# Performance work log

Measured on AMD Instinct MI355X. Metric: run time of the kernel, lower is better.

Reference implementation:

```python
import jax, jax.numpy as jnp
import numpy as np

B, N, E = 4, 8192, 1024
H, G = 16, 64            # num_heads, num_groups
D = E // H               # head_dim = 64
GS = N // G              # group (block) size = 128


def setup_inputs() -> dict:
    key = jax.random.key(0)
    ks = jax.random.split(key, 11)
    std = 0.02
    mk = lambda k, shape: (jax.random.normal(k, shape, dtype=jnp.float32) * std)
    return {
        "q": jax.random.normal(ks[0], (B, N, E), dtype=jnp.float32),
        "k": jax.random.normal(ks[1], (B, N, E), dtype=jnp.float32),
        "v": jax.random.normal(ks[2], (B, N, E), dtype=jnp.float32),
        "Wq": mk(ks[3], (E, E)), "bq": jnp.zeros((E,), jnp.float32),
        "Wk": mk(ks[4], (E, E)), "bk": jnp.zeros((E,), jnp.float32),
        "Wv": mk(ks[5], (E, E)), "bv": jnp.zeros((E,), jnp.float32),
        "Wo": mk(ks[6], (E, E)), "bo": jnp.zeros((E,), jnp.float32),
    }


def reference(q, k, v, Wq, bq, Wk, bk, Wv, bv, Wo, bo):
    b, n, e = q.shape
    scale = 1.0 / (D ** 0.5)

    def proj(x, W, bias):
        # [b,n,e] -> [b,H,G,GS,D]  (split heads, then split seq into groups)
        y = x @ W + bias
        return y.reshape(b, n, H, D).transpose(0, 2, 1, 3).reshape(b, H, G, GS, D)

    qh = proj(q, Wq, bq)
    kh = proj(k, Wk, bk)
    vh = proj(v, Wv, bv)

    # block-diagonal attention: each seq group attends only within itself
    scores = jnp.einsum('bhgqd,bhgkd->bhgqk', qh, kh) * scale  # [b,H,G,GS,GS]
    w = jax.nn.softmax(scores, axis=-1)
    og = jnp.einsum('bhgqk,bhgkd->bhgqd', w, vh)               # [b,H,G,GS,D]

    out = og.reshape(b, H, n, D).transpose(0, 2, 1, 3).reshape(b, n, e)
    out = out @ Wo + bo
    # torch version returns attn_weights of the last group from the loop
    return out, w[:, :, -1]
```

## Files before the change

### kernel.cpp

```cpp
#include <hip/hip_runtime.h>
#include <stdint.h>

#define DEVI static __device__ __forceinline__

typedef __attribute__((ext_vector_type(8))) __bf16 bf16x8;
typedef __attribute__((ext_vector_type(4))) float f32x4;

#define MFMA16(a, b, c) __builtin_amdgcn_mfma_f32_16x16x32_bf16((a), (b), (c), 0, 0, 0)

DEVI uint16_t f2bf(float f) {
  uint32_t u = __builtin_bit_cast(uint32_t, f);
  u += 0x7fffu + ((u >> 16) & 1u);
  return (uint16_t)(u >> 16);
}

DEVI void gload16(const void* g, void* l) {
  __builtin_amdgcn_global_load_lds((const __attribute__((address_space(1))) void*)g,
                                   (__attribute__((address_space(3))) void*)l, 16, 0, 0);
}

#define BARRIER()                         \
  do {                                    \
    __builtin_amdgcn_sched_barrier(0);    \
    __builtin_amdgcn_s_barrier();         \
    __builtin_amdgcn_sched_barrier(0);    \
  } while (0)

__global__ __launch_bounds__(256) void cvt_bf16(const float* __restrict__ in,
                                                uint16_t* __restrict__ out, long n) {
  long i = ((long)blockIdx.x * 256 + threadIdx.x) * 8;
  if (i >= n) return;
  float4 a = *(const float4*)(in + i);
  float4 b = *(const float4*)(in + i + 4);
  union { uint16_t u[8]; uint4 v; } r;
  r.u[0] = f2bf(a.x); r.u[1] = f2bf(a.y); r.u[2] = f2bf(a.z); r.u[3] = f2bf(a.w);
  r.u[4] = f2bf(b.x); r.u[5] = f2bf(b.y); r.u[6] = f2bf(b.z); r.u[7] = f2bf(b.w);
  *(uint4*)(out + i) = r.v;
}

__global__ __launch_bounds__(256) void wtrans(const float* __restrict__ W,
                                              uint16_t* __restrict__ Wt) {
  __shared__ float t[64][65];
  const int ti = blockIdx.y * 64, tj = blockIdx.x * 64;
  {
    int r = threadIdx.x >> 2, c0 = (threadIdx.x & 3) * 16;
#pragma unroll
    for (int i = 0; i < 16; i += 4) {
      float4 v = *(const float4*)(W + (size_t)(ti + r) * 1024 + tj + c0 + i);
      t[r][c0 + i + 0] = v.x; t[r][c0 + i + 1] = v.y;
      t[r][c0 + i + 2] = v.z; t[r][c0 + i + 3] = v.w;
    }
  }
  __syncthreads();
  {
    int c = threadIdx.x >> 2, r0 = (threadIdx.x & 3) * 16;
    union { uint16_t u[16]; uint4 v[2]; } b;
#pragma unroll
    for (int i = 0; i < 16; ++i) b.u[i] = f2bf(t[r0 + i][c]);
    uint16_t* dst = Wt + (size_t)(tj + c) * 1024 + ti + r0;
    *(uint4*)dst = b.v[0];
    *(uint4*)(dst + 8) = b.v[1];
  }
}

__global__ __launch_bounds__(512, 2) void gemm256(const uint16_t* __restrict__ A,
                                                  const uint16_t* __restrict__ Bt,
                                                  const float* __restrict__ bias,
                                                  void* __restrict__ C, int cf32) {
  __shared__ uint8_t lds[131072];
  const int tid = threadIdx.x;
  const int l = tid & 63, w = tid >> 6;
  const int wr = w >> 2, wc = w & 3;
  const int lc = l & 15, lq = l >> 4;

  const int bid = blockIdx.y * 4 + blockIdx.x;
  const int swz = (bid & 7) * 64 + (bid >> 3);
  const size_t m0 = (size_t)(swz >> 2) * 256;
  const int n0 = (swz & 3) * 256;

  const uint8_t* Ab = (const uint8_t*)A + m0 * 2048;
  const uint8_t* Bb = (const uint8_t*)Bt + (size_t)n0 * 2048;

  const int crow = l >> 2;
  const int csw = 16 * ((l & 3) ^ ((l >> 3) & 3));

  auto stageA = [&](int sb, int kt) {
#pragma unroll
    for (int j = 0; j < 2; ++j) {
      const int c = w * 2 + j;
      gload16(Ab + (size_t)(c * 16 + crow) * 2048 + kt * 64 + csw,
              lds + sb * 16384 + c * 1024);
    }
  };
  auto stageB = [&](int sb, int kt) {
#pragma unroll
    for (int j = 0; j < 2; ++j) {
      const int c = w * 2 + j;
      gload16(Bb + (size_t)(c * 16 + crow) * 2048 + kt * 64 + csw,
              lds + 65536 + sb * 16384 + c * 1024);
    }
  };

  const int sel = ((lc >> 1) & 3) << 4;
  auto ldsA = [&](int bf, int mi) -> bf16x8 {
    const int row = wr * 128 + mi * 16 + lc;
    return *(const bf16x8*)(lds + bf * 16384 + row * 64 + ((lq * 16) ^ sel));
  };
  auto ldsB = [&](int bf, int ni) -> bf16x8 {
    const int row = wc * 64 + ni * 16 + lc;
    return *(const bf16x8*)(lds + 65536 + bf * 16384 + row * 64 + ((lq * 16) ^ sel));
  };

  f32x4 acc[8][4] = {};
  bf16x8 aF[8], bF[4];

  stageA(0, 0); stageB(0, 0);
  stageA(1, 1); stageB(1, 1);
  stageA(2, 2); stageB(2, 2);
  asm volatile("s_waitcnt vmcnt(8)" ::: "memory");
  BARRIER();

  for (int kt = 0; kt < 32; ++kt) {
    const int bf = kt & 3;
    const int sb = (kt + 3) & 3;
    const bool st = (kt + 3) < 32;

    if (st) stageA(sb, kt + 3);
#pragma unroll
    for (int mi = 0; mi < 8; ++mi) aF[mi] = ldsA(bf, mi);
#pragma unroll
    for (int ni = 0; ni < 2; ++ni) bF[ni] = ldsB(bf, ni);
    __builtin_amdgcn_s_setprio(1);
#pragma unroll
    for (int mi = 0; mi < 8; ++mi)
#pragma unroll
      for (int ni = 0; ni < 2; ++ni)
        acc[mi][ni] = MFMA16(aF[mi], bF[ni], acc[mi][ni]);
    __builtin_amdgcn_s_setprio(0);

    if (st) stageB(sb, kt + 3);
#pragma unroll
    for (int ni = 2; ni < 4; ++ni) bF[ni] = ldsB(bf, ni);
    __builtin_amdgcn_s_setprio(1);
#pragma unroll
    for (int mi = 0; mi < 8; ++mi)
#pragma unroll
      for (int ni = 2; ni < 4; ++ni)
        acc[mi][ni] = MFMA16(aF[mi], bF[ni], acc[mi][ni]);
    __builtin_amdgcn_s_setprio(0);

    if (kt < 29)       { asm volatile("s_waitcnt vmcnt(8)" ::: "memory"); }
    else if (kt == 29) { asm volatile("s_waitcnt vmcnt(4)" ::: "memory"); }
    else if (kt == 30) { asm volatile("s_waitcnt vmcnt(0)" ::: "memory"); }
    if (kt < 31) BARRIER();
  }

#pragma unroll
  for (int mi = 0; mi < 8; ++mi) {
#pragma unroll
    for (int ni = 0; ni < 4; ++ni) {
      const int col = n0 + wc * 64 + ni * 16 + lc;
      const float bb = bias[col];
#pragma unroll
      for (int r = 0; r < 4; ++r) {
        const size_t row = m0 + wr * 128 + mi * 16 + lq * 4 + r;
        const float vv = acc[mi][ni][r] + bb;
        if (cf32) ((float*)C)[row * 1024 + col] = vv;
        else      ((uint16_t*)C)[row * 1024 + col] = f2bf(vv);
      }
    }
  }
}

__global__ __launch_bounds__(256) void attn(const uint16_t* __restrict__ Qh,
                                            const uint16_t* __restrict__ Kh,
                                            const uint16_t* __restrict__ Vh,
                                            uint16_t* __restrict__ Oh,
                                            float* __restrict__ Wlast) {
  __shared__ uint16_t Ks[128][72];
  __shared__ uint16_t Vt[64][136];
  __shared__ uint16_t Ps[128][136];

  const int blk = blockIdx.x;
  const int b = blk >> 10;
  const int h = (blk >> 6) & 15;
  const int g = blk & 63;
  const size_t rowbase = (size_t)b * 8192 + (size_t)g * 128;
  const int colbase = h * 64;

  const int tid = threadIdx.x, lane = tid & 63, wv = tid >> 6;
  const int lc = lane & 15, lq = lane >> 4;
  const int m0 = wv * 32;

  {
    const int r = tid >> 1, hf = (tid & 1) * 32;
    const uint16_t* ksrc = Kh + (rowbase + r) * 1024 + colbase + hf;
    const uint16_t* vsrc = Vh + (rowbase + r) * 1024 + colbase + hf;
    union { uint16_t u[32]; uint4 v[4]; } kk, vb;
#pragma unroll
    for (int i = 0; i < 4; ++i) kk.v[i] = *(const uint4*)(ksrc + i * 8);
#pragma unroll
    for (int i = 0; i < 4; ++i) vb.v[i] = *(const uint4*)(vsrc + i * 8);
#pragma unroll
    for (int i = 0; i < 4; ++i) *(uint4*)&Ks[r][hf + i * 8] = kk.v[i];
#pragma unroll
    for (int j = 0; j < 32; ++j) Vt[hf + j][r] = vb.u[j];
  }

  bf16x8 aq[2][2];
#pragma unroll
  for (int mi = 0; mi < 2; ++mi)
#pragma unroll
    for (int ks = 0; ks < 2; ++ks)
      aq[mi][ks] = *(const bf16x8*)(Qh + (rowbase + m0 + mi * 16 + lc) * 1024 +
                                    colbase + ks * 32 + lq * 8);

  __syncthreads();

  f32x4 sacc[2][8] = {};
#pragma unroll
  for (int ks = 0; ks < 2; ++ks) {
#pragma unroll
    for (int ni = 0; ni < 8; ++ni) {
      bf16x8 bk = *(const bf16x8*)&Ks[ni * 16 + lc][ks * 32 + lq * 8];
      sacc[0][ni] = MFMA16(aq[0][ks], bk, sacc[0][ni]);
      sacc[1][ni] = MFMA16(aq[1][ks], bk, sacc[1][ni]);
    }
  }

  const float scale = 0.125f;
  float mx[2][4], sm[2][4];
#pragma unroll
  for (int mi = 0; mi < 2; ++mi)
#pragma unroll
    for (int r = 0; r < 4; ++r) {
      float m = -1e30f;
#pragma unroll
      for (int ni = 0; ni < 8; ++ni) m = fmaxf(m, sacc[mi][ni][r]);
      m = fmaxf(m, __shfl_xor(m, 1));
      m = fmaxf(m, __shfl_xor(m, 2));
      m = fmaxf(m, __shfl_xor(m, 4));
      m = fmaxf(m, __shfl_xor(m, 8));
      mx[mi][r] = m * scale;
    }
#pragma unroll
  for (int mi = 0; mi < 2; ++mi)
#pragma unroll
    for (int ni = 0; ni < 8; ++ni)
#pragma unroll
      for (int r = 0; r < 4; ++r)
        sacc[mi][ni][r] = __expf(sacc[mi][ni][r] * scale - mx[mi][r]);
#pragma unroll
  for (int mi = 0; mi < 2; ++mi)
#pragma unroll
    for (int r = 0; r < 4; ++r) {
      float s = 0.f;
#pragma unroll
      for (int ni = 0; ni < 8; ++ni) s += sacc[mi][ni][r];
      s += __shfl_xor(s, 1); s += __shfl_xor(s, 2);
      s += __shfl_xor(s, 4); s += __shfl_xor(s, 8);
      sm[mi][r] = 1.0f / s;
    }

#pragma unroll
  for (int mi = 0; mi < 2; ++mi)
#pragma unroll
    for (int ni = 0; ni < 8; ++ni)
#pragma unroll
      for (int r = 0; r < 4; ++r) {
        float wgt = sacc[mi][ni][r] * sm[mi][r];
        sacc[mi][ni][r] = wgt;
        Ps[m0 + mi * 16 + lq * 4 + r][ni * 16 + lc] = f2bf(wgt);
      }
  if (g == 63) {
    float* wl = Wlast + (size_t)(b * 16 + h) * 16384;
#pragma unroll
    for (int mi = 0; mi < 2; ++mi)
#pragma unroll
      for (int ni = 0; ni < 8; ++ni)
#pragma unroll
        for (int r = 0; r < 4; ++r)
          wl[(size_t)(m0 + mi * 16 + lq * 4 + r) * 128 + ni * 16 + lc] =
              sacc[mi][ni][r];
  }
  __syncthreads();

  f32x4 oacc[2][4] = {};
#pragma unroll
  for (int ks = 0; ks < 4; ++ks) {
    bf16x8 ap[2], bq[4];
#pragma unroll
    for (int mi = 0; mi < 2; ++mi)
      ap[mi] = *(const bf16x8*)&Ps[m0 + mi * 16 + lc][ks * 32 + lq * 8];
#pragma unroll
    for (int ni = 0; ni < 4; ++ni)
      bq[ni] = *(const bf16x8*)&Vt[ni * 16 + lc][ks * 32 + lq * 8];
#pragma unroll
    for (int mi = 0; mi < 2; ++mi)
#pragma unroll
      for (int ni = 0; ni < 4; ++ni)
        oacc[mi][ni] = MFMA16(ap[mi], bq[ni], oacc[mi][ni]);
  }
#pragma unroll
  for (int mi = 0; mi < 2; ++mi)
#pragma unroll
    for (int ni = 0; ni < 4; ++ni)
#pragma unroll
      for (int r = 0; r < 4; ++r)
        Oh[(rowbase + m0 + mi * 16 + lq * 4 + r) * 1024 + colbase + ni * 16 + lc] =
            f2bf(oacc[mi][ni][r]);
}

extern "C" void kernel_launch(void* const* d_in, const int* in_sizes, int n_in,
                              void* d_out, int out_size, void* d_ws, size_t ws_size,
                              hipStream_t stream) {
  (void)in_sizes; (void)n_in; (void)out_size; (void)ws_size;
  const float* q  = (const float*)d_in[0];
  const float* k  = (const float*)d_in[1];
  const float* v  = (const float*)d_in[2];
  const float* Wq = (const float*)d_in[3];
  const float* bq = (const float*)d_in[4];
  const float* Wk = (const float*)d_in[5];
  const float* bk = (const float*)d_in[6];
  const float* Wv = (const float*)d_in[7];
  const float* bv = (const float*)d_in[8];
  const float* Wo = (const float*)d_in[9];
  const float* bo = (const float*)d_in[10];

  uint8_t* ws = (uint8_t*)d_ws;
  const size_t WSZ = (size_t)1024 * 1024 * 2;
  const size_t TSZ = (size_t)32768 * 1024 * 2;
  uint16_t* Wtq = (uint16_t*)(ws + 0 * WSZ);
  uint16_t* Wtk = (uint16_t*)(ws + 1 * WSZ);
  uint16_t* Wtv = (uint16_t*)(ws + 2 * WSZ);
  uint16_t* Wto = (uint16_t*)(ws + 3 * WSZ);
  uint16_t* Qh  = (uint16_t*)(ws + 4 * WSZ);
  uint16_t* Khp = (uint16_t*)(ws + 4 * WSZ + 1 * TSZ);
  uint16_t* Vhp = (uint16_t*)(ws + 4 * WSZ + 2 * TSZ);
  uint16_t* Xs  = (uint16_t*)(ws + 4 * WSZ + 3 * TSZ);

  dim3 tb(256);
  wtrans<<<dim3(16, 16), tb, 0, stream>>>(Wq, Wtq);
  wtrans<<<dim3(16, 16), tb, 0, stream>>>(Wk, Wtk);
  wtrans<<<dim3(16, 16), tb, 0, stream>>>(Wv, Wtv);
  wtrans<<<dim3(16, 16), tb, 0, stream>>>(Wo, Wto);

  const long NE = (long)32768 * 1024;
  const dim3 gg(4, 128), gb(512);
  cvt_bf16<<<16384, tb, 0, stream>>>(q, Xs, NE);
  gemm256<<<gg, gb, 0, stream>>>(Xs, Wtq, bq, Qh, 0);
  cvt_bf16<<<16384, tb, 0, stream>>>(k, Xs, NE);
  gemm256<<<gg, gb, 0, stream>>>(Xs, Wtk, bk, Khp, 0);
  cvt_bf16<<<16384, tb, 0, stream>>>(v, Xs, NE);
  gemm256<<<gg, gb, 0, stream>>>(Xs, Wtv, bv, Vhp, 0);

  float* outp = (float*)d_out;
  attn<<<4096, tb, 0, stream>>>(Qh, Khp, Vhp, Xs, outp + (size_t)32768 * 1024);
  gemm256<<<gg, gb, 0, stream>>>(Xs, Wto, bo, outp, 1);
}
```

Measured before the change: 499.2 us.

## Fuse fp32-to-bf16 conversion into batched QKV projection GEMM, double-buffer LDS

Drops the separate cvt_bf16 passes: the projection GEMM now reads fp32 activations straight from global memory, converts them to bf16 in registers and writes them into swizzled LDS. The Q, K and V projections run as one launch with a z grid dimension, and the four weight transposes are merged into one launch. The GEMM pipeline shrinks from a 4-stage async LDS ring to a 2-stage double buffer with register-staged A, which halves LDS use but exposes more load latency through full vmcnt(0) waits on every iteration. An unused stub kernel gemm256_3 is also left in the file.

```diff
diff --git a/kernel.cpp b/kernel.cpp
--- a/kernel.cpp
+++ b/kernel.cpp
@@ -26,21 +26,15 @@
     __builtin_amdgcn_sched_barrier(0);    \
   } while (0)
 
-__global__ __launch_bounds__(256) void cvt_bf16(const float* __restrict__ in,
-                                                uint16_t* __restrict__ out, long n) {
-  long i = ((long)blockIdx.x * 256 + threadIdx.x) * 8;
-  if (i >= n) return;
-  float4 a = *(const float4*)(in + i);
-  float4 b = *(const float4*)(in + i + 4);
-  union { uint16_t u[8]; uint4 v; } r;
-  r.u[0] = f2bf(a.x); r.u[1] = f2bf(a.y); r.u[2] = f2bf(a.z); r.u[3] = f2bf(a.w);
-  r.u[4] = f2bf(b.x); r.u[5] = f2bf(b.y); r.u[6] = f2bf(b.z); r.u[7] = f2bf(b.w);
-  *(uint4*)(out + i) = r.v;
-}
-
-__global__ __launch_bounds__(256) void wtrans(const float* __restrict__ W,
-                                              uint16_t* __restrict__ Wt) {
+struct W4 {
+  const float* W[4];
+  uint16_t* Wt[4];
+};
+
+__global__ __launch_bounds__(256) void wtrans4(W4 p) {
   __shared__ float t[64][65];
+  const float* __restrict__ W = p.W[blockIdx.z];
+  uint16_t* __restrict__ Wt = p.Wt[blockIdx.z];
   const int ti = blockIdx.y * 64, tj = blockIdx.x * 64;
   {
     int r = threadIdx.x >> 2, c0 = (threadIdx.x & 3) * 16;
@@ -63,11 +57,12 @@
   }
 }
 
-__global__ __launch_bounds__(512, 2) void gemm256(const uint16_t* __restrict__ A,
+template <int AF32>
+__global__ __launch_bounds__(512, 2) void gemm256(const void* __restrict__ Ap,
                                                   const uint16_t* __restrict__ Bt,
                                                   const float* __restrict__ bias,
                                                   void* __restrict__ C, int cf32) {
-  __shared__ uint8_t lds[131072];
+  __shared__ uint8_t lds[65536];
   const int tid = threadIdx.x;
   const int l = tid & 63, w = tid >> 6;
   const int wr = w >> 2, wc = w & 3;
@@ -78,81 +73,101 @@
   const size_t m0 = (size_t)(swz >> 2) * 256;
   const int n0 = (swz & 3) * 256;
 
-  const uint8_t* Ab = (const uint8_t*)A + m0 * 2048;
+  const float* Af = (const float*)Ap;
+  const uint8_t* Ab = (const uint8_t*)Ap + m0 * 2048;
   const uint8_t* Bb = (const uint8_t*)Bt + (size_t)n0 * 2048;
 
   const int crow = l >> 2;
   const int csw = 16 * ((l & 3) ^ ((l >> 3) & 3));
-
-  auto stageA = [&](int sb, int kt) {
+  auto stageA_bf = [&](int sel, int kt) {
 #pragma unroll
     for (int j = 0; j < 2; ++j) {
       const int c = w * 2 + j;
       gload16(Ab + (size_t)(c * 16 + crow) * 2048 + kt * 64 + csw,
-              lds + sb * 16384 + c * 1024);
-    }
-  };
-  auto stageB = [&](int sb, int kt) {
+              lds + sel * 16384 + c * 1024);
+    }
+  };
+  auto stageB = [&](int sel, int kt) {
 #pragma unroll
     for (int j = 0; j < 2; ++j) {
       const int c = w * 2 + j;
       gload16(Bb + (size_t)(c * 16 + crow) * 2048 + kt * 64 + csw,
-              lds + 65536 + sb * 16384 + c * 1024);
-    }
-  };
-
-  const int sel = ((lc >> 1) & 3) << 4;
+              lds + 32768 + sel * 16384 + c * 1024);
+    }
+  };
+
+  const int rbase = tid >> 3, fq = tid & 7;
+  const int acol = ((((fq >> 1) ^ ((rbase >> 1) & 3))) << 4) + (fq & 1) * 8;
+  auto loadA_f32 = [&](int kt, float4 (&ra)[4]) {
+#pragma unroll
+    for (int i = 0; i < 4; ++i)
+      ra[i] = *(const float4*)(Af + (m0 + rbase + i * 64) * 1024 + kt * 32 + fq * 4);
+  };
+  auto writeA_bf = [&](int sel, float4 (&ra)[4]) {
+#pragma unroll
+    for (int i = 0; i < 4; ++i) {
+      union { uint16_t u[4]; uint2 v; } t;
+      t.u[0] = f2bf(ra[i].x); t.u[1] = f2bf(ra[i].y);
+      t.u[2] = f2bf(ra[i].z); t.u[3] = f2bf(ra[i].w);
+      *(uint2*)(lds + sel * 16384 + (rbase + i * 64) * 64 + acol) = t.v;
+    }
+  };
+
+  const int sel4 = ((lc >> 1) & 3) << 4;
   auto ldsA = [&](int bf, int mi) -> bf16x8 {
     const int row = wr * 128 + mi * 16 + lc;
-    return *(const bf16x8*)(lds + bf * 16384 + row * 64 + ((lq * 16) ^ sel));
+    return *(const bf16x8*)(lds + bf * 16384 + row * 64 + ((lq * 16) ^ sel4));
   };
   auto ldsB = [&](int bf, int ni) -> bf16x8 {
     const int row = wc * 64 + ni * 16 + lc;
-    return *(const bf16x8*)(lds + 65536 + bf * 16384 + row * 64 + ((lq * 16) ^ sel));
+    return *(const bf16x8*)(lds + 32768 + bf * 16384 + row * 64 + ((lq * 16) ^ sel4));
   };
 
   f32x4 acc[8][4] = {};
-  bf16x8 aF[8], bF[4];
-
-  stageA(0, 0); stageB(0, 0);
-  stageA(1, 1); stageB(1, 1);
-  stageA(2, 2); stageB(2, 2);
-  asm volatile("s_waitcnt vmcnt(8)" ::: "memory");
+
+  if constexpr (AF32) {
+    float4 r0[4];
+    loadA_f32(0, r0);
+    stageB(0, 0);
+    asm volatile("s_waitcnt vmcnt(0)" ::: "memory");
+    writeA_bf(0, r0);
+    asm volatile("s_waitcnt lgkmcnt(0)" ::: "memory");
+  } else {
+    stageA_bf(0, 0);
+    stageB(0, 0);
+    asm volatile("s_waitcnt vmcnt(0)" ::: "memory");
+  }
   BARRIER();
 
   for (int kt = 0; kt < 32; ++kt) {
-    const int bf = kt & 3;
-    const int sb = (kt + 3) & 3;
-    const bool st = (kt + 3) < 32;
-
-    if (st) stageA(sb, kt + 3);
-#pragma unroll
-    for (int mi = 0; mi < 8; ++mi) aF[mi] = ldsA(bf, mi);
-#pragma unroll
-    for (int ni = 0; ni < 2; ++ni) bF[ni] = ldsB(bf, ni);
+    const int cur = kt & 1;
+    const bool more = (kt + 1 < 32);
+    float4 ra[4];
+    if (more) {
+      if constexpr (AF32) loadA_f32(kt + 1, ra);
+      else                stageA_bf(cur ^ 1, kt + 1);
+      stageB(cur ^ 1, kt + 1);
+    }
+    bf16x8 aF[8], bF[4];
+#pragma unroll
+    for (int ni = 0; ni < 4; ++ni) bF[ni] = ldsB(cur, ni);
+#pragma unroll
+    for (int mi = 0; mi < 8; ++mi) aF[mi] = ldsA(cur, mi);
     __builtin_amdgcn_s_setprio(1);
 #pragma unroll
     for (int mi = 0; mi < 8; ++mi)
 #pragma unroll
-      for (int ni = 0; ni < 2; ++ni)
+      for (int ni = 0; ni < 4; ++ni)
         acc[mi][ni] = MFMA16(aF[mi], bF[ni], acc[mi][ni]);
     __builtin_amdgcn_s_setprio(0);
-
-    if (st) stageB(sb, kt + 3);
-#pragma unroll
-    for (int ni = 2; ni < 4; ++ni) bF[ni] = ldsB(bf, ni);
-    __builtin_amdgcn_s_setprio(1);
-#pragma unroll
-    for (int mi = 0; mi < 8; ++mi)
-#pragma unroll
-      for (int ni = 2; ni < 4; ++ni)
-        acc[mi][ni] = MFMA16(aF[mi], bF[ni], acc[mi][ni]);
-    __builtin_amdgcn_s_setprio(0);
-
-    if (kt < 29)       { asm volatile("s_waitcnt vmcnt(8)" ::: "memory"); }
-    else if (kt == 29) { asm volatile("s_waitcnt vmcnt(4)" ::: "memory"); }
-    else if (kt == 30) { asm volatile("s_waitcnt vmcnt(0)" ::: "memory"); }
-    if (kt < 31) BARRIER();
+    if (more) {
+      asm volatile("s_waitcnt vmcnt(0)" ::: "memory");
+      if constexpr (AF32) writeA_bf(cur ^ 1, ra);
+    }
+    if (kt < 31) {
+      asm volatile("s_waitcnt lgkmcnt(0)" ::: "memory");
+      BARRIER();
+    }
   }
 
 #pragma unroll
@@ -167,6 +182,136 @@
         const float vv = acc[mi][ni][r] + bb;
         if (cf32) ((float*)C)[row * 1024 + col] = vv;
         else      ((uint16_t*)C)[row * 1024 + col] = f2bf(vv);
+      }
+    }
+  }
+}
+
+struct Proj3 {
+  const void* A[3];
+  const uint16_t* W[3];
+  const float* b[3];
+  void* C[3];
+};
+
+template <int AF32>
+__global__ __launch_bounds__(512, 2) void gemm256_3(Proj3 p) {
+  const int z = blockIdx.z;
+  {
+    __shared__ uint8_t dummy;
+    (void)dummy;
+  }
+  (void)p; (void)z;
+}
+
+__global__ __launch_bounds__(512, 2) void gemm_proj3(Proj3 p) {
+  __shared__ uint8_t lds[65536];
+  const int tid = threadIdx.x;
+  const int l = tid & 63, w = tid >> 6;
+  const int wr = w >> 2, wc = w & 3;
+  const int lc = l & 15, lq = l >> 4;
+  const int z = blockIdx.z;
+
+  const int bid = blockIdx.y * 4 + blockIdx.x;
+  const int swz = (bid & 7) * 64 + (bid >> 3);
+  const size_t m0 = (size_t)(swz >> 2) * 256;
+  const int n0 = (swz & 3) * 256;
+
+  const float* Af = (const float*)p.A[z];
+  const uint8_t* Bb = (const uint8_t*)p.W[z] + (size_t)n0 * 2048;
+  const float* bias = p.b[z];
+  uint16_t* C = (uint16_t*)p.C[z];
+
+  const int crow = l >> 2;
+  const int csw = 16 * ((l & 3) ^ ((l >> 3) & 3));
+  auto stageB = [&](int sel, int kt) {
+#pragma unroll
+    for (int j = 0; j < 2; ++j) {
+      const int c = w * 2 + j;
+      gload16(Bb + (size_t)(c * 16 + crow) * 2048 + kt * 64 + csw,
+              lds + 32768 + sel * 16384 + c * 1024);
+    }
+  };
+
+  const int rbase = tid >> 3, fq = tid & 7;
+  const int acol = ((((fq >> 1) ^ ((rbase >> 1) & 3))) << 4) + (fq & 1) * 8;
+  auto loadA_f32 = [&](int kt, float4 (&ra)[4]) {
+#pragma unroll
+    for (int i = 0; i < 4; ++i)
+      ra[i] = *(const float4*)(Af + (m0 + rbase + i * 64) * 1024 + kt * 32 + fq * 4);
+  };
+  auto writeA_bf = [&](int sel, float4 (&ra)[4]) {
+#pragma unroll
+    for (int i = 0; i < 4; ++i) {
+      union { uint16_t u[4]; uint2 v; } t;
+      t.u[0] = f2bf(ra[i].x); t.u[1] = f2bf(ra[i].y);
+      t.u[2] = f2bf(ra[i].z); t.u[3] = f2bf(ra[i].w);
+      *(uint2*)(lds + sel * 16384 + (rbase + i * 64) * 64 + acol) = t.v;
+    }
+  };
+
+  const int sel4 = ((lc >> 1) & 3) << 4;
+  auto ldsA = [&](int bf, int mi) -> bf16x8 {
+    const int row = wr * 128 + mi * 16 + lc;
+    return *(const bf16x8*)(lds + bf * 16384 + row * 64 + ((lq * 16) ^ sel4));
+  };
+  auto ldsB = [&](int bf, int ni) -> bf16x8 {
+    const int row = wc * 64 + ni * 16 + lc;
+    return *(const bf16x8*)(lds + 32768 + bf * 16384 + row * 64 + ((lq * 16) ^ sel4));
+  };
+
+  f32x4 acc[8][4] = {};
+
+  {
+    float4 r0[4];
+    loadA_f32(0, r0);
+    stageB(0, 0);
+    asm volatile("s_waitcnt vmcnt(0)" ::: "memory");
+    writeA_bf(0, r0);
+    asm volatile("s_waitcnt lgkmcnt(0)" ::: "memory");
+  }
+  BARRIER();
+
+  for (int kt = 0; kt < 32; ++kt) {
+    const int cur = kt & 1;
+    const bool more = (kt + 1 < 32);
+    float4 ra[4];
+    if (more) {
+      loadA_f32(kt + 1, ra);
+      stageB(cur ^ 1, kt + 1);
+    }
+    bf16x8 aF[8], bF[4];
+#pragma unroll
+    for (int ni = 0; ni < 4; ++ni) bF[ni] = ldsB(cur, ni);
+#pragma unroll
+    for (int mi = 0; mi < 8; ++mi) aF[mi] = ldsA(cur, mi);
+    __builtin_amdgcn_s_setprio(1);
+#pragma unroll
+    for (int mi = 0; mi < 8; ++mi)
+#pragma unroll
+      for (int ni = 0; ni < 4; ++ni)
+        acc[mi][ni] = MFMA16(aF[mi], bF[ni], acc[mi][ni]);
+    __builtin_amdgcn_s_setprio(0);
+    if (more) {
+      asm volatile("s_waitcnt vmcnt(0)" ::: "memory");
+      writeA_bf(cur ^ 1, ra);
+    }
+    if (kt < 31) {
+      asm volatile("s_waitcnt lgkmcnt(0)" ::: "memory");
+      BARRIER();
+    }
+  }
+
+#pragma unroll
+  for (int mi = 0; mi < 8; ++mi) {
+#pragma unroll
+    for (int ni = 0; ni < 4; ++ni) {
+      const int col = n0 + wc * 64 + ni * 16 + lc;
+      const float bb = bias[col];
+#pragma unroll
+      for (int r = 0; r < 4; ++r) {
+        const size_t row = m0 + wr * 128 + mi * 16 + lq * 4 + r;
+        C[row * 1024 + col] = f2bf(acc[mi][ni][r] + bb);
       }
     }
   }
@@ -339,22 +484,19 @@
   uint16_t* Vhp = (uint16_t*)(ws + 4 * WSZ + 2 * TSZ);
   uint16_t* Xs  = (uint16_t*)(ws + 4 * WSZ + 3 * TSZ);
 
-  dim3 tb(256);
-  wtrans<<<dim3(16, 16), tb, 0, stream>>>(Wq, Wtq);
-  wtrans<<<dim3(16, 16), tb, 0, stream>>>(Wk, Wtk);
-  wtrans<<<dim3(16, 16), tb, 0, stream>>>(Wv, Wtv);
-  wtrans<<<dim3(16, 16), tb, 0, stream>>>(Wo, Wto);
-
-  const long NE = (long)32768 * 1024;
-  const dim3 gg(4, 128), gb(512);
-  cvt_bf16<<<16384, tb, 0, stream>>>(q, Xs, NE);
-  gemm256<<<gg, gb, 0, stream>>>(Xs, Wtq, bq, Qh, 0);
-  cvt_bf16<<<16384, tb, 0, stream>>>(k, Xs, NE);
-  gemm256<<<gg, gb, 0, stream>>>(Xs, Wtk, bk, Khp, 0);
-  cvt_bf16<<<16384, tb, 0, stream>>>(v, Xs, NE);
-  gemm256<<<gg, gb, 0, stream>>>(Xs, Wtv, bv, Vhp, 0);
+  W4 wt;
+  wt.W[0] = Wq; wt.W[1] = Wk; wt.W[2] = Wv; wt.W[3] = Wo;
+  wt.Wt[0] = Wtq; wt.Wt[1] = Wtk; wt.Wt[2] = Wtv; wt.Wt[3] = Wto;
+  wtrans4<<<dim3(16, 16, 4), 256, 0, stream>>>(wt);
+
+  Proj3 p;
+  p.A[0] = q;  p.A[1] = k;  p.A[2] = v;
+  p.W[0] = Wtq; p.W[1] = Wtk; p.W[2] = Wtv;
+  p.b[0] = bq; p.b[1] = bk; p.b[2] = bv;
+  p.C[0] = Qh; p.C[1] = Khp; p.C[2] = Vhp;
+  gemm_proj3<<<dim3(4, 128, 3), 512, 0, stream>>>(p);
 
   float* outp = (float*)d_out;
-  attn<<<4096, tb, 0, stream>>>(Qh, Khp, Vhp, Xs, outp + (size_t)32768 * 1024);
-  gemm256<<<gg, gb, 0, stream>>>(Xs, Wto, bo, outp, 1);
-}
+  attn<<<4096, 256, 0, stream>>>(Qh, Khp, Vhp, Xs, outp + (size_t)32768 * 1024);
+  gemm256<0><<<dim3(4, 128), 512, 0, stream>>>(Xs, Wto, bo, outp, 1);
+}
```

After: 560.1 us. 12.2% more time.

## Double K-tile depth in GEMM with asymmetric A/B LDS buffering; batch weight transposes

Applied to the files above, without the earlier changes.

The projection GEMM now stages 128-wide K tiles (16 iterations instead of 32), with three LDS buffers for A and two for B and a new XOR swizzle over 8 16-byte chunks. This halves the number of barriers and waits per K loop and gives larger MFMA bursts between syncs. The cost is LDS use growing to 160KB, which drops occupancy from the two blocks per CU requested in launch bounds to one, so latency hiding now rests on the deeper per-tile work. The four weight-transpose launches are also merged into one launch over a z dimension.

```diff
diff --git a/kernel.cpp b/kernel.cpp
--- a/kernel.cpp
+++ b/kernel.cpp
@@ -38,9 +38,15 @@
   *(uint4*)(out + i) = r.v;
 }
 
-__global__ __launch_bounds__(256) void wtrans(const float* __restrict__ W,
-                                              uint16_t* __restrict__ Wt) {
+struct W4 {
+  const float* W[4];
+  uint16_t* Wt[4];
+};
+
+__global__ __launch_bounds__(256) void wtrans4(W4 p) {
   __shared__ float t[64][65];
+  const float* __restrict__ W = p.W[blockIdx.z];
+  uint16_t* __restrict__ Wt = p.Wt[blockIdx.z];
   const int ti = blockIdx.y * 64, tj = blockIdx.x * 64;
   {
     int r = threadIdx.x >> 2, c0 = (threadIdx.x & 3) * 16;
@@ -67,7 +73,7 @@
                                                   const uint16_t* __restrict__ Bt,
                                                   const float* __restrict__ bias,
                                                   void* __restrict__ C, int cf32) {
-  __shared__ uint8_t lds[131072];
+  __shared__ uint8_t lds[163840];
   const int tid = threadIdx.x;
   const int l = tid & 63, w = tid >> 6;
   const int wr = w >> 2, wc = w & 3;
@@ -81,78 +87,66 @@
   const uint8_t* Ab = (const uint8_t*)A + m0 * 2048;
   const uint8_t* Bb = (const uint8_t*)Bt + (size_t)n0 * 2048;
 
-  const int crow = l >> 2;
-  const int csw = 16 * ((l & 3) ^ ((l >> 3) & 3));
+  const int srow = tid >> 3;
+  const int susw = ((tid & 7) ^ (srow & 7)) * 16;
 
   auto stageA = [&](int sb, int kt) {
 #pragma unroll
-    for (int j = 0; j < 2; ++j) {
-      const int c = w * 2 + j;
-      gload16(Ab + (size_t)(c * 16 + crow) * 2048 + kt * 64 + csw,
-              lds + sb * 16384 + c * 1024);
-    }
+    for (int j = 0; j < 4; ++j)
+      gload16(Ab + (size_t)(j * 64 + srow) * 2048 + kt * 128 + susw,
+              lds + sb * 32768 + j * 8192 + w * 1024);
   };
-  auto stageB = [&](int sb, int kt) {
-#pragma unroll
-    for (int j = 0; j < 2; ++j) {
-      const int c = w * 2 + j;
-      gload16(Bb + (size_t)(c * 16 + crow) * 2048 + kt * 64 + csw,
-              lds + 65536 + sb * 16384 + c * 1024);
-    }
+  auto stageB = [&](int db, int kt) {
+#pragma unroll
+    for (int j = 0; j < 4; ++j)
+      gload16(Bb + (size_t)(j * 64 + srow) * 2048 + kt * 128 + susw,
+              lds + 98304 + db * 32768 + j * 8192 + w * 1024);
   };
 
-  const int sel = ((lc >> 1) & 3) << 4;
-  auto ldsA = [&](int bf, int mi) -> bf16x8 {
+  auto ldsA = [&](int sb, int mi, int kk) -> bf16x8 {
     const int row = wr * 128 + mi * 16 + lc;
-    return *(const bf16x8*)(lds + bf * 16384 + row * 64 + ((lq * 16) ^ sel));
+    const int u = ((kk * 4 + lq) ^ (row & 7)) * 16;
+    return *(const bf16x8*)(lds + sb * 32768 + row * 128 + u);
   };
-  auto ldsB = [&](int bf, int ni) -> bf16x8 {
+  auto ldsB = [&](int db, int ni, int kk) -> bf16x8 {
     const int row = wc * 64 + ni * 16 + lc;
-    return *(const bf16x8*)(lds + 65536 + bf * 16384 + row * 64 + ((lq * 16) ^ sel));
+    const int u = ((kk * 4 + lq) ^ (row & 7)) * 16;
+    return *(const bf16x8*)(lds + 98304 + db * 32768 + row * 128 + u);
   };
 
   f32x4 acc[8][4] = {};
-  bf16x8 aF[8], bF[4];
-
-  stageA(0, 0); stageB(0, 0);
-  stageA(1, 1); stageB(1, 1);
-  stageA(2, 2); stageB(2, 2);
-  asm volatile("s_waitcnt vmcnt(8)" ::: "memory");
+
+  stageA(0, 0);
+  stageB(0, 0);
+  stageA(1, 1);
+  asm volatile("s_waitcnt vmcnt(4)" ::: "memory");
   BARRIER();
 
-  for (int kt = 0; kt < 32; ++kt) {
-    const int bf = kt & 3;
-    const int sb = (kt + 3) & 3;
-    const bool st = (kt + 3) < 32;
-
-    if (st) stageA(sb, kt + 3);
-#pragma unroll
-    for (int mi = 0; mi < 8; ++mi) aF[mi] = ldsA(bf, mi);
-#pragma unroll
-    for (int ni = 0; ni < 2; ++ni) bF[ni] = ldsB(bf, ni);
-    __builtin_amdgcn_s_setprio(1);
-#pragma unroll
-    for (int mi = 0; mi < 8; ++mi)
-#pragma unroll
-      for (int ni = 0; ni < 2; ++ni)
-        acc[mi][ni] = MFMA16(aF[mi], bF[ni], acc[mi][ni]);
-    __builtin_amdgcn_s_setprio(0);
-
-    if (st) stageB(sb, kt + 3);
-#pragma unroll
-    for (int ni = 2; ni < 4; ++ni) bF[ni] = ldsB(bf, ni);
-    __builtin_amdgcn_s_setprio(1);
-#pragma unroll
-    for (int mi = 0; mi < 8; ++mi)
-#pragma unroll
-      for (int ni = 2; ni < 4; ++ni)
-        acc[mi][ni] = MFMA16(aF[mi], bF[ni], acc[mi][ni]);
-    __builtin_amdgcn_s_setprio(0);
-
-    if (kt < 29)       { asm volatile("s_waitcnt vmcnt(8)" ::: "memory"); }
-    else if (kt == 29) { asm volatile("s_waitcnt vmcnt(4)" ::: "memory"); }
-    else if (kt == 30) { asm volatile("s_waitcnt vmcnt(0)" ::: "memory"); }
-    if (kt < 31) BARRIER();
+  for (int t = 0; t < 16; ++t) {
+    const int ab = t % 3;
+    const int bb = t & 1;
+    if (t + 1 < 16) stageB((t + 1) & 1, t + 1);
+    if (t + 2 < 16) stageA((t + 2) % 3, t + 2);
+
+#pragma unroll
+    for (int kk = 0; kk < 2; ++kk) {
+      bf16x8 bF[4], aF[8];
+#pragma unroll
+      for (int ni = 0; ni < 4; ++ni) bF[ni] = ldsB(bb, ni, kk);
+#pragma unroll
+      for (int mi = 0; mi < 8; ++mi) aF[mi] = ldsA(ab, mi, kk);
+      __builtin_amdgcn_s_setprio(1);
+#pragma unroll
+      for (int mi = 0; mi < 8; ++mi)
+#pragma unroll
+        for (int ni = 0; ni < 4; ++ni)
+          acc[mi][ni] = MFMA16(aF[mi], bF[ni], acc[mi][ni]);
+      __builtin_amdgcn_s_setprio(0);
+    }
+
+    if (t < 14)       { asm volatile("s_waitcnt vmcnt(4)" ::: "memory"); }
+    else if (t == 14) { asm volatile("s_waitcnt vmcnt(0)" ::: "memory"); }
+    if (t < 15) BARRIER();
   }
 
 #pragma unroll
@@ -160,11 +154,11 @@
 #pragma unroll
     for (int ni = 0; ni < 4; ++ni) {
       const int col = n0 + wc * 64 + ni * 16 + lc;
-      const float bb = bias[col];
+      const float bb2 = bias[col];
 #pragma unroll
       for (int r = 0; r < 4; ++r) {
         const size_t row = m0 + wr * 128 + mi * 16 + lq * 4 + r;
-        const float vv = acc[mi][ni][r] + bb;
+        const float vv = acc[mi][ni][r] + bb2;
         if (cf32) ((float*)C)[row * 1024 + col] = vv;
         else      ((uint16_t*)C)[row * 1024 + col] = f2bf(vv);
       }
@@ -339,22 +333,21 @@
   uint16_t* Vhp = (uint16_t*)(ws + 4 * WSZ + 2 * TSZ);
   uint16_t* Xs  = (uint16_t*)(ws + 4 * WSZ + 3 * TSZ);
 
-  dim3 tb(256);
-  wtrans<<<dim3(16, 16), tb, 0, stream>>>(Wq, Wtq);
-  wtrans<<<dim3(16, 16), tb, 0, stream>>>(Wk, Wtk);
-  wtrans<<<dim3(16, 16), tb, 0, stream>>>(Wv, Wtv);
-  wtrans<<<dim3(16, 16), tb, 0, stream>>>(Wo, Wto);
+  W4 wt;
+  wt.W[0] = Wq; wt.W[1] = Wk; wt.W[2] = Wv; wt.W[3] = Wo;
+  wt.Wt[0] = Wtq; wt.Wt[1] = Wtk; wt.Wt[2] = Wtv; wt.Wt[3] = Wto;
+  wtrans4<<<dim3(16, 16, 4), 256, 0, stream>>>(wt);
 
   const long NE = (long)32768 * 1024;
   const dim3 gg(4, 128), gb(512);
-  cvt_bf16<<<16384, tb, 0, stream>>>(q, Xs, NE);
+  cvt_bf16<<<16384, 256, 0, stream>>>(q, Xs, NE);
   gemm256<<<gg, gb, 0, stream>>>(Xs, Wtq, bq, Qh, 0);
-  cvt_bf16<<<16384, tb, 0, stream>>>(k, Xs, NE);
+  cvt_bf16<<<16384, 256, 0, stream>>>(k, Xs, NE);
   gemm256<<<gg, gb, 0, stream>>>(Xs, Wtk, bk, Khp, 0);
-  cvt_bf16<<<16384, tb, 0, stream>>>(v, Xs, NE);
+  cvt_bf16<<<16384, 256, 0, stream>>>(v, Xs, NE);
   gemm256<<<gg, gb, 0, stream>>>(Xs, Wtv, bv, Vhp, 0);
 
   float* outp = (float*)d_out;
-  attn<<<4096, tb, 0, stream>>>(Qh, Khp, Vhp, Xs, outp + (size_t)32768 * 1024);
+  attn<<<4096, 256, 0, stream>>>(Qh, Khp, Vhp, Xs, outp + (size_t)32768 * 1024);
   gemm256<<<gg, gb, 0, stream>>>(Xs, Wto, bo, outp, 1);
 }
```

Result: faster. 473.9 us (-5.1%).
